# Kernel optimization log

Hardware: AMD Instinct MI355X
Metric: run time of the kernel (lower is better)

Reference implementation:

```python
import jax, jax.numpy as jnp
import numpy as np

B = 4_194_304
N_LJ = 3      # hp.n_lj
N_GAUSS = 4   # hp.n_gauss


def setup_inputs() -> dict:
    key = jax.random.key(0)
    k1, k2 = jax.random.split(key)
    # distances in [1, 4] Angstrom to keep inverse powers well-behaved
    distance = jax.random.uniform(k1, (B,), dtype=jnp.float32) * 3.0 + 1.0
    # per-sample params: 3 LJ triplets (m, c, sigma) + 4 Gaussian triplets
    # (amplitude, mean, stddev); keep in [0.5, 1.0] so sigma/stddev != 0
    lj_gauss_param = jax.random.uniform(k2, (B, 21), dtype=jnp.float32) * 0.5 + 0.5
    return {"distance": distance, "lj_gauss_param": lj_gauss_param}


def reference(distance, lj_gauss_param):
    # distance: [B], lj_gauss_param: [B, 21]
    d = distance[:, None]                                   # [B, 1]

    # --- Lennard-Jones terms (first 9 params -> [B, 3, 3]; m unused) ---
    lj = lj_gauss_param[:, : 3 * N_LJ].reshape(-1, N_LJ, 3)
    c = lj[..., 1]
    sigma = lj[..., 2]
    inv_r = sigma / d                                       # [B, 3]
    inv_r6 = inv_r ** 6
    inv_r12 = inv_r6 * inv_r6
    lj_energy = 4.0 * c * (inv_r12 - inv_r6)
    lj_force = -4.0 * c * (4.0 * sigma ** 6 / d ** 7 - 12.0 * sigma ** 12 / d ** 13)

    # --- Gaussian terms (last 12 params -> [B, 4, 3]) ---
    g = lj_gauss_param[:, 3 * N_LJ : 3 * N_LJ + 3 * N_GAUSS].reshape(-1, N_GAUSS, 3)
    amplitude = g[..., 0]
    mean = g[..., 1]
    stddev = g[..., 2]
    dm = d - mean                                           # [B, 4]
    exp_term = jnp.exp(-(dm ** 2) / (2.0 * stddev ** 2))
    gauss_energy = amplitude * exp_term
    gauss_force = -(amplitude * dm * exp_term * dm ** 2 / stddev ** 2) / stddev ** 2

    energies = lj_energy.sum(axis=-1) + gauss_energy.sum(axis=-1)   # [B]
    forces = lj_force.sum(axis=-1) + gauss_force.sum(axis=-1)       # [B]
    return energies, forces
```

## Files before the change

kernel.cpp:

```cpp
#include <hip/hip_runtime.h>


constexpr int BLOCK = 256;
constexpr int NPAR  = 21;
constexpr int NV4   = BLOCK * NPAR / 4;

__global__ __launch_bounds__(BLOCK)
void gauslj_kernel(const float* __restrict__ distance,
                   const float* __restrict__ param,
                   float* __restrict__ out,
                   int n)
{
    __shared__ float4 sp4[NV4];
    float* sp = (float*)sp4;

    const int t = threadIdx.x;
    const long long base = (long long)blockIdx.x * BLOCK;

    if (base + BLOCK <= n) {
        const float4* g4 = (const float4*)(param + base * NPAR);
        const int wbase = t & ~63;
        #pragma unroll
        for (int j = 0; j < 6; ++j) {
            const int idx = j * 256 + t;
            if (idx < NV4) {
                __builtin_amdgcn_global_load_lds(
                    (const __attribute__((address_space(1))) void*)(g4 + idx),
                    (__attribute__((address_space(3))) void*)(sp4 + j * 256 + wbase),
                    16, 0, 0);
            }
        }
    } else {
        const long long gbase  = base * NPAR;
        const long long ptotal = (long long)n * NPAR;
        for (int j = 0; j < NPAR; ++j) {
            long long g = gbase + j * BLOCK + t;
            if (g < ptotal) sp[j * BLOCK + t] = param[g];
        }
    }
    __syncthreads();

    const long long i = base + t;
    if (i >= n) return;

    const float d     = distance[i];
    const float inv_d = __builtin_amdgcn_rcpf(d);
    const float id2   = inv_d * inv_d;
    const float id4   = id2 * id2;
    const float id6   = id4 * id2;
    const float id7   = id6 * inv_d;
    const float id12  = id6 * id6;
    const float id13  = id12 * inv_d;

    const float* p = &sp[t * NPAR];

    float e = 0.0f, f = 0.0f;

    #pragma unroll
    for (int k = 0; k < 3; ++k) {
        const float c   = p[3 * k + 1];
        const float s   = p[3 * k + 2];
        const float s2  = s * s;
        const float s6  = s2 * s2 * s2;
        const float s12 = s6 * s6;
        e += 4.0f * c * (s12 * id12 - s6 * id6);
        f += -4.0f * c * (4.0f * s6 * id7 - 12.0f * s12 * id13);
    }

    #pragma unroll
    for (int k = 0; k < 4; ++k) {
        const float a       = p[9 + 3 * k + 0];
        const float mu      = p[9 + 3 * k + 1];
        const float sd      = p[9 + 3 * k + 2];
        const float dm      = d - mu;
        const float inv_sd2 = __builtin_amdgcn_rcpf(sd * sd);
        const float ex      = __expf(-0.5f * dm * dm * inv_sd2);
        e += a * ex;
        f += -(a * dm * ex) * (dm * dm) * inv_sd2 * inv_sd2;
    }

    __builtin_nontemporal_store(e, &out[i]);
    __builtin_nontemporal_store(f, &out[n + i]);
}

extern "C" void kernel_launch(void* const* d_in, const int* in_sizes, int n_in,
                              void* d_out, int out_size, void* d_ws, size_t ws_size,
                              hipStream_t stream) {
    const float* distance = (const float*)d_in[0];
    const float* param    = (const float*)d_in[1];
    float* out            = (float*)d_out;
    const int n = in_sizes[0];

    const int grid = (n + BLOCK - 1) / BLOCK;
    gauslj_kernel<<<grid, BLOCK, 0, stream>>>(distance, param, out, n);
}
```

Baseline: 76.76 us.

## Use persistent grid with double-buffered LDS prefetch of parameter tiles

Replaces the one-block-per-tile launch with a fixed grid of 768 persistent blocks that loop over tiles. The next tile's parameters are prefetched into a second LDS buffer with global_load_lds while the current tile is computed. This is meant to overlap memory traffic with compute and cut per-block launch overhead. The trade-off is twice the LDS per block (about 43KB), which lowers occupancy, plus a barrier each iteration. There is also a sync hazard: nothing visibly waits on the asynchronous LDS loads before the barrier.

After: 79.17 us. +3.1%, slower.

```diff
diff --git a/kernel.cpp b/kernel.cpp
--- a/kernel.cpp
+++ b/kernel.cpp
@@ -1,86 +1,105 @@
 #include <hip/hip_runtime.h>
 
 
-constexpr int BLOCK = 256;
-constexpr int NPAR  = 21;
-constexpr int NV4   = BLOCK * NPAR / 4;
+constexpr int BLOCK   = 256;
+constexpr int NPAR    = 21;
+constexpr int TILE_F4 = BLOCK * NPAR / 4;
+constexpr int GRID    = 768;
 
-__global__ __launch_bounds__(BLOCK)
+__device__ __forceinline__ void stage_tile(float4* dst, const float* __restrict__ param,
+                                           long long base, int n, int t)
+{
+    if (base + BLOCK <= (long long)n) {
+        const float4* g4 = (const float4*)(param + base * NPAR);
+        const int wbase = t & ~63;
+        #pragma unroll
+        for (int j = 0; j < 6; ++j) {
+            const int idx = j * 256 + t;
+            if (idx < TILE_F4) {
+                __builtin_amdgcn_global_load_lds(
+                    (const __attribute__((address_space(1))) void*)(g4 + idx),
+                    (__attribute__((address_space(3))) void*)(dst + j * 256 + wbase),
+                    16, 0, 0);
+            }
+        }
+    } else {
+        float* d = (float*)dst;
+        const long long gbase = base * NPAR;
+        const long long ptot  = (long long)n * NPAR;
+        for (int j = 0; j < NPAR; ++j) {
+            long long g = gbase + j * BLOCK + t;
+            if (g < ptot) d[j * BLOCK + t] = param[g];
+        }
+    }
+}
+
+__global__ __launch_bounds__(BLOCK, 3)
 void gauslj_kernel(const float* __restrict__ distance,
                    const float* __restrict__ param,
                    float* __restrict__ out,
                    int n)
 {
-    __shared__ float4 sp4[NV4];
-    float* sp = (float*)sp4;
+    __shared__ float4 buf[2][TILE_F4];
 
     const int t = threadIdx.x;
-    const long long base = (long long)blockIdx.x * BLOCK;
+    const int T = (n + BLOCK - 1) / BLOCK;
 
-    if (base + BLOCK <= n) {
-        const float4* g4 = (const float4*)(param + base * NPAR);
-        const int wbase = t & ~63;
+    int tile = blockIdx.x;
+    if (tile >= T) return;
+
+    stage_tile(buf[0], param, (long long)tile * BLOCK, n, t);
+    int cur = 0;
+
+    for (; tile < T; tile += GRID) {
+        __syncthreads();
+        const long long base = (long long)tile * BLOCK;
+        const long long i    = base + t;
+        const float d = (i < n) ? distance[i] : 1.0f;
+
+        const int nxt = tile + GRID;
+        if (nxt < T)
+            stage_tile(buf[cur ^ 1], param, (long long)nxt * BLOCK, n, t);
+
+        const float inv_d = __builtin_amdgcn_rcpf(d);
+        const float id2   = inv_d * inv_d;
+        const float id6   = id2 * id2 * id2;
+        const float id7   = id6 * inv_d;
+        const float id12  = id6 * id6;
+        const float id13  = id12 * inv_d;
+
+        const float* p = (const float*)buf[cur] + t * NPAR;
+
+        float e = 0.0f, f = 0.0f;
+
         #pragma unroll
-        for (int j = 0; j < 6; ++j) {
-            const int idx = j * 256 + t;
-            if (idx < NV4) {
-                __builtin_amdgcn_global_load_lds(
-                    (const __attribute__((address_space(1))) void*)(g4 + idx),
-                    (__attribute__((address_space(3))) void*)(sp4 + j * 256 + wbase),
-                    16, 0, 0);
-            }
+        for (int k = 0; k < 3; ++k) {
+            const float c   = p[3 * k + 1];
+            const float s   = p[3 * k + 2];
+            const float s2  = s * s;
+            const float s6  = s2 * s2 * s2;
+            const float s12 = s6 * s6;
+            e += 4.0f * c * (s12 * id12 - s6 * id6);
+            f += -4.0f * c * (4.0f * s6 * id7 - 12.0f * s12 * id13);
         }
-    } else {
-        const long long gbase  = base * NPAR;
-        const long long ptotal = (long long)n * NPAR;
-        for (int j = 0; j < NPAR; ++j) {
-            long long g = gbase + j * BLOCK + t;
-            if (g < ptotal) sp[j * BLOCK + t] = param[g];
+
+        #pragma unroll
+        for (int k = 0; k < 4; ++k) {
+            const float a       = p[9 + 3 * k + 0];
+            const float mu      = p[9 + 3 * k + 1];
+            const float sd      = p[9 + 3 * k + 2];
+            const float dm      = d - mu;
+            const float inv_sd2 = __builtin_amdgcn_rcpf(sd * sd);
+            const float ex      = __expf(-0.5f * dm * dm * inv_sd2);
+            e += a * ex;
+            f += -(a * dm * ex) * (dm * dm) * inv_sd2 * inv_sd2;
         }
+
+        if (i < n) {
+            __builtin_nontemporal_store(e, &out[i]);
+            __builtin_nontemporal_store(f, &out[n + i]);
+        }
+        cur ^= 1;
     }
-    __syncthreads();
-
-    const long long i = base + t;
-    if (i >= n) return;
-
-    const float d     = distance[i];
-    const float inv_d = __builtin_amdgcn_rcpf(d);
-    const float id2   = inv_d * inv_d;
-    const float id4   = id2 * id2;
-    const float id6   = id4 * id2;
-    const float id7   = id6 * inv_d;
-    const float id12  = id6 * id6;
-    const float id13  = id12 * inv_d;
-
-    const float* p = &sp[t * NPAR];
-
-    float e = 0.0f, f = 0.0f;
-
-    #pragma unroll
-    for (int k = 0; k < 3; ++k) {
-        const float c   = p[3 * k + 1];
-        const float s   = p[3 * k + 2];
-        const float s2  = s * s;
-        const float s6  = s2 * s2 * s2;
-        const float s12 = s6 * s6;
-        e += 4.0f * c * (s12 * id12 - s6 * id6);
-        f += -4.0f * c * (4.0f * s6 * id7 - 12.0f * s12 * id13);
-    }
-
-    #pragma unroll
-    for (int k = 0; k < 4; ++k) {
-        const float a       = p[9 + 3 * k + 0];
-        const float mu      = p[9 + 3 * k + 1];
-        const float sd      = p[9 + 3 * k + 2];
-        const float dm      = d - mu;
-        const float inv_sd2 = __builtin_amdgcn_rcpf(sd * sd);
-        const float ex      = __expf(-0.5f * dm * dm * inv_sd2);
-        e += a * ex;
-        f += -(a * dm * ex) * (dm * dm) * inv_sd2 * inv_sd2;
-    }
-
-    __builtin_nontemporal_store(e, &out[i]);
-    __builtin_nontemporal_store(f, &out[n + i]);
 }
 
 extern "C" void kernel_launch(void* const* d_in, const int* in_sizes, int n_in,
@@ -91,6 +110,7 @@
     float* out            = (float*)d_out;
     const int n = in_sizes[0];
 
-    const int grid = (n + BLOCK - 1) / BLOCK;
+    const int T = (n + BLOCK - 1) / BLOCK;
+    const int grid = (T < GRID) ? T : GRID;
     gauslj_kernel<<<grid, BLOCK, 0, stream>>>(distance, param, out, n);
 }
```

## Replace LDS staging with per-thread float4 register loads of 4 samples

Applied to the files above, without the earlier changes.

Drops the shared-memory staging of the parameter rows through global_load_lds. Each thread now processes four consecutive samples and loads their 84 parameters straight into registers with 21 float4 loads. Distance loads and output stores become float4 vectors as well. Per-thread loads are strided by 336 bytes across lanes, so coalescing is worse than the block-wide contiguous LDS copy, and register pressure goes up.

Measured after the change: 122.0 us. 1.59x slower.

```diff
diff --git a/kernel.cpp b/kernel.cpp
--- a/kernel.cpp
+++ b/kernel.cpp
@@ -1,60 +1,23 @@
 #include <hip/hip_runtime.h>
 
 
+typedef float f32x4 __attribute__((ext_vector_type(4)));
+
 constexpr int BLOCK = 256;
 constexpr int NPAR  = 21;
-constexpr int NV4   = BLOCK * NPAR / 4;
+constexpr int EPT   = 4;
 
-__global__ __launch_bounds__(BLOCK)
-void gauslj_kernel(const float* __restrict__ distance,
-                   const float* __restrict__ param,
-                   float* __restrict__ out,
-                   int n)
+__device__ __forceinline__ void compute_one(float d, const float* __restrict__ p,
+                                            float& e, float& f)
 {
-    __shared__ float4 sp4[NV4];
-    float* sp = (float*)sp4;
-
-    const int t = threadIdx.x;
-    const long long base = (long long)blockIdx.x * BLOCK;
-
-    if (base + BLOCK <= n) {
-        const float4* g4 = (const float4*)(param + base * NPAR);
-        const int wbase = t & ~63;
-        #pragma unroll
-        for (int j = 0; j < 6; ++j) {
-            const int idx = j * 256 + t;
-            if (idx < NV4) {
-                __builtin_amdgcn_global_load_lds(
-                    (const __attribute__((address_space(1))) void*)(g4 + idx),
-                    (__attribute__((address_space(3))) void*)(sp4 + j * 256 + wbase),
-                    16, 0, 0);
-            }
-        }
-    } else {
-        const long long gbase  = base * NPAR;
-        const long long ptotal = (long long)n * NPAR;
-        for (int j = 0; j < NPAR; ++j) {
-            long long g = gbase + j * BLOCK + t;
-            if (g < ptotal) sp[j * BLOCK + t] = param[g];
-        }
-    }
-    __syncthreads();
-
-    const long long i = base + t;
-    if (i >= n) return;
-
-    const float d     = distance[i];
     const float inv_d = __builtin_amdgcn_rcpf(d);
     const float id2   = inv_d * inv_d;
-    const float id4   = id2 * id2;
-    const float id6   = id4 * id2;
+    const float id6   = id2 * id2 * id2;
     const float id7   = id6 * inv_d;
     const float id12  = id6 * id6;
     const float id13  = id12 * inv_d;
 
-    const float* p = &sp[t * NPAR];
-
-    float e = 0.0f, f = 0.0f;
+    e = 0.0f; f = 0.0f;
 
     #pragma unroll
     for (int k = 0; k < 3; ++k) {
@@ -78,9 +41,50 @@
         e += a * ex;
         f += -(a * dm * ex) * (dm * dm) * inv_sd2 * inv_sd2;
     }
+}
 
-    __builtin_nontemporal_store(e, &out[i]);
-    __builtin_nontemporal_store(f, &out[n + i]);
+__global__ __launch_bounds__(BLOCK)
+void gauslj_kernel(const float* __restrict__ distance,
+                   const float* __restrict__ param,
+                   float* __restrict__ out,
+                   int n)
+{
+    const long long gid = (long long)blockIdx.x * BLOCK + threadIdx.x;
+    const long long i0  = gid * EPT;
+    if (i0 >= n) return;
+
+    if (i0 + EPT <= n) {
+        const f32x4* p4 = (const f32x4*)(param + i0 * NPAR);
+        float pv[EPT * NPAR];
+        #pragma unroll
+        for (int j = 0; j < NPAR; ++j) {
+            const f32x4 v = p4[j];
+            pv[4 * j + 0] = v.x; pv[4 * j + 1] = v.y;
+            pv[4 * j + 2] = v.z; pv[4 * j + 3] = v.w;
+        }
+        const f32x4 dv = *(const f32x4*)(distance + i0);
+        const float de[EPT] = {dv.x, dv.y, dv.z, dv.w};
+
+        f32x4 eo, fo;
+        float ev[EPT], fv[EPT];
+        #pragma unroll
+        for (int e = 0; e < EPT; ++e)
+            compute_one(de[e], &pv[e * NPAR], ev[e], fv[e]);
+        eo.x = ev[0]; eo.y = ev[1]; eo.z = ev[2]; eo.w = ev[3];
+        fo.x = fv[0]; fo.y = fv[1]; fo.z = fv[2]; fo.w = fv[3];
+
+        __builtin_nontemporal_store(eo, (f32x4*)(out + i0));
+        __builtin_nontemporal_store(fo, (f32x4*)(out + n + i0));
+    } else {
+        for (long long i = i0; i < n; ++i) {
+            float pv[NPAR];
+            for (int j = 0; j < NPAR; ++j) pv[j] = param[i * NPAR + j];
+            float e, f;
+            compute_one(distance[i], pv, e, f);
+            out[i]     = e;
+            out[n + i] = f;
+        }
+    }
 }
 
 extern "C" void kernel_launch(void* const* d_in, const int* in_sizes, int n_in,
@@ -91,6 +95,7 @@
     float* out            = (float*)d_out;
     const int n = in_sizes[0];
 
-    const int grid = (n + BLOCK - 1) / BLOCK;
+    const long long threads = ((long long)n + EPT - 1) / EPT;
+    const int grid = (int)((threads + BLOCK - 1) / BLOCK);
     gauslj_kernel<<<grid, BLOCK, 0, stream>>>(distance, param, out, n);
 }
```
